# Kernel tuning notes

Hardware: AMD Instinct MI355X
Metric: run time of the kernel (lower is better)

Reference implementation:

```python
import jax, jax.numpy as jnp
import numpy as np

TEMPERATURE = 0.07
EPS = 1e-12


def setup_inputs() -> dict:
    key = jax.random.key(0)
    k1, k2 = jax.random.split(key)
    B, D = 16384, 256
    return {
        "query_embeds": jax.random.normal(k1, (B, D), dtype=jnp.float32),
        "database_embeds": jax.random.normal(k2, (B, D), dtype=jnp.float32),
    }


def _l2_normalize(x, axis=1):
    # torch F.normalize: x / max(||x||, eps)
    norm = jnp.sqrt(jnp.sum(x * x, axis=axis, keepdims=True))
    return x / jnp.maximum(norm, EPS)


def reference(query_embeds, database_embeds):
    q = _l2_normalize(query_embeds, axis=1)   # [B, D]
    d = _l2_normalize(database_embeds, axis=1)  # [B, D]
    sim = jnp.einsum("bd,cd->bc", q, d) / TEMPERATURE  # [B, B]
    B = sim.shape[0]
    diag = jnp.diagonal(sim)  # logits at the correct (matching) label
    # CE over rows (q->d): -log_softmax(sim, axis=1)[i, i]
    lse_rows = jax.nn.logsumexp(sim, axis=1)
    loss_q2d = jnp.mean(lse_rows - diag)
    # CE over rows of sim.T == columns of sim (d->q)
    lse_cols = jax.nn.logsumexp(sim, axis=0)
    loss_d2q = jnp.mean(lse_cols - diag)
    return (loss_q2d + loss_d2q) / 2
```

## Files before the change

### kernel.cpp

```cpp
#include <hip/hip_runtime.h>
#include <hip/hip_bf16.h>
#include <cstdint>
#include <cstddef>

#define B_ROWS 16384
#define D_DIM  256
#define TEMP_INV 14.285714285714286f

#define NITER 16

using frag_cd = __attribute__((ext_vector_type(4))) float;
using i32x4   = __attribute__((ext_vector_type(4))) int;
using i32x8   = __attribute__((ext_vector_type(8))) int;

__device__ __forceinline__ void gld_lds16(const void* g, void* l) {
    __builtin_amdgcn_global_load_lds(
        (const __attribute__((address_space(1))) void*)g,
        (__attribute__((address_space(3))) void*)l,
        16, 0, 0);
}


__global__ __launch_bounds__(256) void norm_diag_kernel(
    const float* __restrict__ q, const float* __restrict__ d,
    unsigned int* __restrict__ qn, unsigned int* __restrict__ dn,
    float* __restrict__ diag,
    float* __restrict__ row_sums, float* __restrict__ col_sums,
    float* __restrict__ out) {
    const int b = blockIdx.x;
    if (b < 64)            row_sums[b * 256 + threadIdx.x] = 0.0f;
    else if (b < 128)      col_sums[(b - 64) * 256 + threadIdx.x] = 0.0f;
    else if (b == 128 && threadIdx.x == 0) out[0] = 0.0f;

    const int t    = threadIdx.x;
    const int lane = t & 63;
    const int w    = t >> 6;
    const int l15  = lane & 15;
    const int rw   = lane >> 4;
    const int r    = w * 4 + rw;
    const int row  = b * 16 + r;

    const float4* qr = (const float4*)(q + (size_t)row * D_DIM);
    const float4* dr = (const float4*)(d + (size_t)row * D_DIM);
    float4 qv[4], dv[4];
    float qss = 0.f, dss = 0.f, qd = 0.f;
#pragma unroll
    for (int p = 0; p < 4; ++p) {
        qv[p] = qr[l15 + 16 * p];
        dv[p] = dr[l15 + 16 * p];
        qss += qv[p].x*qv[p].x + qv[p].y*qv[p].y + qv[p].z*qv[p].z + qv[p].w*qv[p].w;
        dss += dv[p].x*dv[p].x + dv[p].y*dv[p].y + dv[p].z*dv[p].z + dv[p].w*dv[p].w;
        qd  += qv[p].x*dv[p].x + qv[p].y*dv[p].y + qv[p].z*dv[p].z + qv[p].w*dv[p].w;
    }
#pragma unroll
    for (int off = 1; off < 16; off <<= 1) {
        qss += __shfl_xor(qss, off);
        dss += __shfl_xor(dss, off);
        qd  += __shfl_xor(qd,  off);
    }
    const float qinv = 1.0f / fmaxf(sqrtf(qss), 1e-12f);
    const float dinv = 1.0f / fmaxf(sqrtf(dss), 1e-12f);

    __shared__ unsigned int qbuf[1024], dbuf[1024];
#pragma unroll
    for (int p = 0; p < 4; ++p) {
        const int jw = l15 + 16 * p;
        int qp = 0, dp = 0;
        qp = __builtin_amdgcn_cvt_pk_fp8_f32(qv[p].x * qinv, qv[p].y * qinv, qp, false);
        qp = __builtin_amdgcn_cvt_pk_fp8_f32(qv[p].z * qinv, qv[p].w * qinv, qp, true);
        dp = __builtin_amdgcn_cvt_pk_fp8_f32(dv[p].x * dinv, dv[p].y * dinv, dp, false);
        dp = __builtin_amdgcn_cvt_pk_fp8_f32(dv[p].z * dinv, dv[p].w * dinv, dp, true);
        const int c    = (jw & 31) >> 2;
        const int widx = ((jw >> 5) << 9) | ((c >> 2) << 8) | ((c & 3) << 6)
                       | (r << 2) | (jw & 3);
        qbuf[widx] = (unsigned int)qp;
        dbuf[widx] = (unsigned int)dp;
    }
    if (l15 == 0) diag[row] = qd * qinv * dinv * TEMP_INV;
    __syncthreads();
    ((uint4*)qn)[(size_t)b * 256 + t] = ((const uint4*)qbuf)[t];
    ((uint4*)dn)[(size_t)b * 256 + t] = ((const uint4*)dbuf)[t];
}

__global__ __launch_bounds__(256, 2) void gemm_lse_kernel(
    const unsigned char* __restrict__ qn, const unsigned char* __restrict__ dn,
    float* __restrict__ row_sums, float* __restrict__ col_sums) {
    __shared__ unsigned char ldsB[3][16384];

    const int t    = threadIdx.x;
    const int lane = t & 63;
    const int w    = t >> 6;
    const int l15  = lane & 15;
    const int quad = lane >> 4;

    const int id   = blockIdx.x;
    const int xcd  = id & 7;
    const int i    = id >> 3;
    const int chunk   = (xcd << 1) | (i & 1);
    const int rowg    = i >> 1;
    const int rowBase = rowg * 256;
    const int colChunkBase = chunk * 1024;

    union OpU { i32x8 v; i32x4 h[2]; };

    const unsigned char* aB = qn + ((size_t)((rowBase >> 4) + w * 4) << 12) + lane * 16;
    OpU a8[4][2];
#pragma unroll
    for (int mi = 0; mi < 4; ++mi)
#pragma unroll
        for (int kt = 0; kt < 2; ++kt) {
            a8[mi][kt].h[0] = *(const i32x4*)(aB + mi * 4096 + kt * 2048);
            a8[mi][kt].h[1] = *(const i32x4*)(aB + mi * 4096 + kt * 2048 + 1024);
        }

    const unsigned char* bG = dn + ((size_t)(colChunkBase >> 4) << 12);

#define STAGE(bufidx, j)                                                      \
    {                                                                          \
        const unsigned char* gsrc = bG + (size_t)(j) * 16384;                  \
        unsigned char* ldst = &ldsB[bufidx][0];                                \
        _Pragma("unroll")                                                      \
        for (int ii = 0; ii < 4; ++ii)                                         \
            gld_lds16(gsrc + ii * 4096 + t * 16, ldst + ii * 4096 + t * 16);   \
    }

    STAGE(0, 0)
    STAGE(1, 1)

    union RV { frag_cd v[4]; float f[16]; } rvu;
#pragma unroll
    for (int k = 0; k < 4; ++k) rvu.v[k] = (frag_cd){0.f, 0.f, 0.f, 0.f};

    const float C2 = TEMP_INV * 1.44269504088896f;

    int cur = 0;
#pragma unroll 1
    for (int it = 0; it < NITER; ++it) {
        if (it == NITER - 1) asm volatile("s_waitcnt vmcnt(0)" ::: "memory");
        else                 asm volatile("s_waitcnt vmcnt(4)" ::: "memory");
        __builtin_amdgcn_s_barrier();
        asm volatile("" ::: "memory");

        const int nxt = (cur + 2 >= 3) ? cur - 1 : cur + 2;
        if (it + 2 < NITER) STAGE(nxt, it + 2)

        const unsigned char* bL = &ldsB[cur][0] + lane * 16;

        frag_cd acc[4][4];
#pragma unroll
        for (int mi = 0; mi < 4; ++mi)
#pragma unroll
            for (int ni = 0; ni < 4; ++ni)
                acc[mi][ni] = (frag_cd){0.f, 0.f, 0.f, 0.f};

        {
            OpU b8[4];
#pragma unroll
            for (int ni = 0; ni < 4; ++ni) {
                b8[ni].h[0] = *(const i32x4*)(bL + ni * 4096);
                b8[ni].h[1] = *(const i32x4*)(bL + ni * 4096 + 1024);
            }
            __builtin_amdgcn_s_setprio(1);
#pragma unroll
            for (int mi = 0; mi < 4; ++mi)
#pragma unroll
                for (int ni = 0; ni < 4; ++ni)
                    acc[mi][ni] = __builtin_amdgcn_mfma_scale_f32_16x16x128_f8f6f4(
                        a8[mi][0].v, b8[ni].v, acc[mi][ni],
                        0, 0, 0, 0x7F7F7F7F, 0, 0x7F7F7F7F);
            __builtin_amdgcn_s_setprio(0);
        }
        {
            OpU b8[4];
#pragma unroll
            for (int ni = 0; ni < 4; ++ni) {
                b8[ni].h[0] = *(const i32x4*)(bL + ni * 4096 + 2048);
                b8[ni].h[1] = *(const i32x4*)(bL + ni * 4096 + 2048 + 1024);
            }
            __builtin_amdgcn_s_setprio(1);
#pragma unroll
            for (int mi = 0; mi < 4; ++mi)
#pragma unroll
                for (int ni = 0; ni < 4; ++ni)
                    acc[mi][ni] = __builtin_amdgcn_mfma_scale_f32_16x16x128_f8f6f4(
                        a8[mi][1].v, b8[ni].v, acc[mi][ni],
                        0, 0, 0, 0x7F7F7F7F, 0, 0x7F7F7F7F);
            __builtin_amdgcn_s_setprio(0);
        }

        frag_cd cv4[4];
#pragma unroll
        for (int k = 0; k < 4; ++k) cv4[k] = (frag_cd){0.f, 0.f, 0.f, 0.f};
#pragma unroll
        for (int mi = 0; mi < 4; ++mi)
#pragma unroll
            for (int ni = 0; ni < 4; ++ni) {
                const frag_cd tt = acc[mi][ni] * C2 - C2;
                frag_cd e;
#pragma unroll
                for (int rr = 0; rr < 4; ++rr) e[rr] = __builtin_amdgcn_exp2f(tt[rr]);
                rvu.v[mi] += e;
                cv4[ni]   += e;
            }
        float cv[4];
#pragma unroll
        for (int ni = 0; ni < 4; ++ni)
            cv[ni] = (cv4[ni][0] + cv4[ni][1]) + (cv4[ni][2] + cv4[ni][3]);

#pragma unroll
        for (int s = 0; s < 2; ++s) {
            const bool bb = (quad >> s) & 1;
#pragma unroll
            for (int k = 0; k < (2 >> s); ++k) {
                const float a0 = cv[2 * k], a1 = cv[2 * k + 1];
                const float keep = bb ? a1 : a0;
                const float send = bb ? a0 : a1;
                cv[k] = keep + __shfl_xor(send, 16 << s);
            }
        }
        atomicAdd(&col_sums[colChunkBase + it * 64 + quad * 16 + l15], cv[0]);

        cur = (cur + 1 >= 3) ? 0 : cur + 1;
    }
#undef STAGE

#pragma unroll
    for (int s = 0; s < 4; ++s) {
        const bool bb = (l15 >> s) & 1;
#pragma unroll
        for (int k = 0; k < (8 >> s); ++k) {
            const float a0 = rvu.f[2 * k], a1 = rvu.f[2 * k + 1];
            const float keep = bb ? a1 : a0;
            const float send = bb ? a0 : a1;
            rvu.f[k] = keep + __shfl_xor(send, 1 << s);
        }
    }
    atomicAdd(&row_sums[rowBase + w * 64 + (l15 >> 2) * 16 + quad * 4 + (l15 & 3)],
              rvu.f[0]);
}

__global__ __launch_bounds__(256) void finalize_kernel(
    const float* __restrict__ rs, const float* __restrict__ cs,
    const float* __restrict__ dg, float* __restrict__ out) {
    const int i = blockIdx.x * 256 + threadIdx.x;
    float s = logf(rs[i]) + logf(cs[i]) - 2.0f * dg[i];
#pragma unroll
    for (int off = 32; off; off >>= 1) s += __shfl_down(s, off);
    __shared__ float buf[4];
    if ((threadIdx.x & 63) == 0) buf[threadIdx.x >> 6] = s;
    __syncthreads();
    if (threadIdx.x == 0) {
        float tot = (buf[0] + buf[1] + buf[2] + buf[3]) / (2.0f * B_ROWS);
        if (blockIdx.x == 0) tot += TEMP_INV;
        atomicAdd(out, tot);
    }
}

extern "C" void kernel_launch(void* const* d_in, const int* in_sizes, int n_in,
                              void* d_out, int out_size, void* d_ws, size_t ws_size,
                              hipStream_t stream) {
    const float* q = (const float*)d_in[0];
    const float* d = (const float*)d_in[1];
    float* out = (float*)d_out;

    char* ws = (char*)d_ws;
    unsigned char* qn = (unsigned char*)ws;
    unsigned char* dn = qn + (size_t)B_ROWS * D_DIM;
    float* row_sums = (float*)(ws + 2 * (size_t)B_ROWS * D_DIM);
    float* col_sums = row_sums + B_ROWS;
    float* diag     = col_sums + B_ROWS;

    norm_diag_kernel<<<B_ROWS / 16, 256, 0, stream>>>(
        q, d, (unsigned int*)qn, (unsigned int*)dn, diag, row_sums, col_sums, out);
    gemm_lse_kernel<<<(B_ROWS / 256) * (B_ROWS / 1024), 256, 0, stream>>>(
        qn, dn, row_sums, col_sums);
    finalize_kernel<<<B_ROWS / 256, 256, 0, stream>>>(row_sums, col_sums, diag, out);
}
```

Before: 149.8 us.

## Halve GEMM row tile, double-buffer LDS, and raise occupancy to four blocks

```diff
diff --git a/kernel.cpp b/kernel.cpp
--- a/kernel.cpp
+++ b/kernel.cpp
@@ -82,10 +82,10 @@
     ((uint4*)dn)[(size_t)b * 256 + t] = ((const uint4*)dbuf)[t];
 }
 
-__global__ __launch_bounds__(256, 2) void gemm_lse_kernel(
+__global__ __launch_bounds__(256, 4) void gemm_lse_kernel(
     const unsigned char* __restrict__ qn, const unsigned char* __restrict__ dn,
     float* __restrict__ row_sums, float* __restrict__ col_sums) {
-    __shared__ unsigned char ldsB[3][16384];
+    __shared__ unsigned char ldsB[2][16384];
 
     const int t    = threadIdx.x;
     const int lane = t & 63;
@@ -98,15 +98,15 @@
     const int i    = id >> 3;
     const int chunk   = (xcd << 1) | (i & 1);
     const int rowg    = i >> 1;
-    const int rowBase = rowg * 256;
+    const int rowBase = rowg * 128;
     const int colChunkBase = chunk * 1024;
 
     union OpU { i32x8 v; i32x4 h[2]; };
 
-    const unsigned char* aB = qn + ((size_t)((rowBase >> 4) + w * 4) << 12) + lane * 16;
-    OpU a8[4][2];
-#pragma unroll
-    for (int mi = 0; mi < 4; ++mi)
+    const unsigned char* aB = qn + ((size_t)((rowBase >> 4) + w * 2) << 12) + lane * 16;
+    OpU a8[2][2];
+#pragma unroll
+    for (int mi = 0; mi < 2; ++mi)
 #pragma unroll
         for (int kt = 0; kt < 2; ++kt) {
             a8[mi][kt].h[0] = *(const i32x4*)(aB + mi * 4096 + kt * 2048);
@@ -125,74 +125,60 @@
     }
 
     STAGE(0, 0)
-    STAGE(1, 1)
-
-    union RV { frag_cd v[4]; float f[16]; } rvu;
-#pragma unroll
-    for (int k = 0; k < 4; ++k) rvu.v[k] = (frag_cd){0.f, 0.f, 0.f, 0.f};
+
+    union RV { frag_cd v[2]; float f[8]; } rvu;
+#pragma unroll
+    for (int k = 0; k < 2; ++k) rvu.v[k] = (frag_cd){0.f, 0.f, 0.f, 0.f};
 
     const float C2 = TEMP_INV * 1.44269504088896f;
+    const frag_cd zf = (frag_cd){0.f, 0.f, 0.f, 0.f};
 
     int cur = 0;
 #pragma unroll 1
     for (int it = 0; it < NITER; ++it) {
-        if (it == NITER - 1) asm volatile("s_waitcnt vmcnt(0)" ::: "memory");
-        else                 asm volatile("s_waitcnt vmcnt(4)" ::: "memory");
+        asm volatile("s_waitcnt vmcnt(0)" ::: "memory");
         __builtin_amdgcn_s_barrier();
         asm volatile("" ::: "memory");
-
-        const int nxt = (cur + 2 >= 3) ? cur - 1 : cur + 2;
-        if (it + 2 < NITER) STAGE(nxt, it + 2)
+        if (it + 1 < NITER) STAGE(cur ^ 1, it + 1)
 
         const unsigned char* bL = &ldsB[cur][0] + lane * 16;
 
-        frag_cd acc[4][4];
-#pragma unroll
-        for (int mi = 0; mi < 4; ++mi)
+        frag_cd acc[2][4];
+        OpU b8[4];
+
+#pragma unroll
+        for (int ni = 0; ni < 4; ++ni) {
+            b8[ni].h[0] = *(const i32x4*)(bL + ni * 4096);
+            b8[ni].h[1] = *(const i32x4*)(bL + ni * 4096 + 1024);
+        }
+        __builtin_amdgcn_s_setprio(1);
+#pragma unroll
+        for (int mi = 0; mi < 2; ++mi)
 #pragma unroll
             for (int ni = 0; ni < 4; ++ni)
-                acc[mi][ni] = (frag_cd){0.f, 0.f, 0.f, 0.f};
-
-        {
-            OpU b8[4];
-#pragma unroll
-            for (int ni = 0; ni < 4; ++ni) {
-                b8[ni].h[0] = *(const i32x4*)(bL + ni * 4096);
-                b8[ni].h[1] = *(const i32x4*)(bL + ni * 4096 + 1024);
-            }
-            __builtin_amdgcn_s_setprio(1);
-#pragma unroll
-            for (int mi = 0; mi < 4; ++mi)
-#pragma unroll
-                for (int ni = 0; ni < 4; ++ni)
-                    acc[mi][ni] = __builtin_amdgcn_mfma_scale_f32_16x16x128_f8f6f4(
-                        a8[mi][0].v, b8[ni].v, acc[mi][ni],
-                        0, 0, 0, 0x7F7F7F7F, 0, 0x7F7F7F7F);
-            __builtin_amdgcn_s_setprio(0);
-        }
-        {
-            OpU b8[4];
-#pragma unroll
-            for (int ni = 0; ni < 4; ++ni) {
-                b8[ni].h[0] = *(const i32x4*)(bL + ni * 4096 + 2048);
-                b8[ni].h[1] = *(const i32x4*)(bL + ni * 4096 + 2048 + 1024);
-            }
-            __builtin_amdgcn_s_setprio(1);
-#pragma unroll
-            for (int mi = 0; mi < 4; ++mi)
-#pragma unroll
-                for (int ni = 0; ni < 4; ++ni)
-                    acc[mi][ni] = __builtin_amdgcn_mfma_scale_f32_16x16x128_f8f6f4(
-                        a8[mi][1].v, b8[ni].v, acc[mi][ni],
-                        0, 0, 0, 0x7F7F7F7F, 0, 0x7F7F7F7F);
-            __builtin_amdgcn_s_setprio(0);
-        }
-
-        frag_cd cv4[4];
-#pragma unroll
-        for (int k = 0; k < 4; ++k) cv4[k] = (frag_cd){0.f, 0.f, 0.f, 0.f};
-#pragma unroll
-        for (int mi = 0; mi < 4; ++mi)
+                acc[mi][ni] = __builtin_amdgcn_mfma_scale_f32_16x16x128_f8f6f4(
+                    a8[mi][0].v, b8[ni].v, zf,
+                    0, 0, 0, 0x7F7F7F7F, 0, 0x7F7F7F7F);
+        __builtin_amdgcn_s_setprio(0);
+
+#pragma unroll
+        for (int ni = 0; ni < 4; ++ni) {
+            b8[ni].h[0] = *(const i32x4*)(bL + ni * 4096 + 2048);
+            b8[ni].h[1] = *(const i32x4*)(bL + ni * 4096 + 2048 + 1024);
+        }
+        __builtin_amdgcn_s_setprio(1);
+#pragma unroll
+        for (int mi = 0; mi < 2; ++mi)
+#pragma unroll
+            for (int ni = 0; ni < 4; ++ni)
+                acc[mi][ni] = __builtin_amdgcn_mfma_scale_f32_16x16x128_f8f6f4(
+                    a8[mi][1].v, b8[ni].v, acc[mi][ni],
+                    0, 0, 0, 0x7F7F7F7F, 0, 0x7F7F7F7F);
+        __builtin_amdgcn_s_setprio(0);
+
+        float cv[4] = {0.f, 0.f, 0.f, 0.f};
+#pragma unroll
+        for (int mi = 0; mi < 2; ++mi)
 #pragma unroll
             for (int ni = 0; ni < 4; ++ni) {
                 const frag_cd tt = acc[mi][ni] * C2 - C2;
@@ -200,12 +186,8 @@
 #pragma unroll
                 for (int rr = 0; rr < 4; ++rr) e[rr] = __builtin_amdgcn_exp2f(tt[rr]);
                 rvu.v[mi] += e;
-                cv4[ni]   += e;
+                cv[ni] += (e[0] + e[1]) + (e[2] + e[3]);
             }
-        float cv[4];
-#pragma unroll
-        for (int ni = 0; ni < 4; ++ni)
-            cv[ni] = (cv4[ni][0] + cv4[ni][1]) + (cv4[ni][2] + cv4[ni][3]);
 
 #pragma unroll
         for (int s = 0; s < 2; ++s) {
@@ -220,23 +202,26 @@
         }
         atomicAdd(&col_sums[colChunkBase + it * 64 + quad * 16 + l15], cv[0]);
 
-        cur = (cur + 1 >= 3) ? 0 : cur + 1;
+        cur ^= 1;
     }
 #undef STAGE
 
 #pragma unroll
-    for (int s = 0; s < 4; ++s) {
+    for (int k = 0; k < 8; ++k) rvu.f[k] += __shfl_xor(rvu.f[k], 8);
+#pragma unroll
+    for (int s = 0; s < 3; ++s) {
         const bool bb = (l15 >> s) & 1;
 #pragma unroll
-        for (int k = 0; k < (8 >> s); ++k) {
+        for (int k = 0; k < (4 >> s); ++k) {
             const float a0 = rvu.f[2 * k], a1 = rvu.f[2 * k + 1];
             const float keep = bb ? a1 : a0;
             const float send = bb ? a0 : a1;
             rvu.f[k] = keep + __shfl_xor(send, 1 << s);
         }
     }
-    atomicAdd(&row_sums[rowBase + w * 64 + (l15 >> 2) * 16 + quad * 4 + (l15 & 3)],
-              rvu.f[0]);
+    if (l15 < 8)
+        atomicAdd(&row_sums[rowBase + w * 32 + ((l15 >> 2) & 1) * 16 + quad * 4
+                            + (l15 & 3)], rvu.f[0]);
 }
 
 __global__ __launch_bounds__(256) void finalize_kernel(
@@ -272,7 +257,7 @@
 
     norm_diag_kernel<<<B_ROWS / 16, 256, 0, stream>>>(
         q, d, (unsigned int*)qn, (unsigned int*)dn, diag, row_sums, col_sums, out);
-    gemm_lse_kernel<<<(B_ROWS / 256) * (B_ROWS / 1024), 256, 0, stream>>>(
+    gemm_lse_kernel<<<(B_ROWS / 128) * (B_ROWS / 1024), 256, 0, stream>>>(
         qn, dn, row_sums, col_sums);
     finalize_kernel<<<B_ROWS / 256, 256, 0, stream>>>(row_sums, col_sums, diag, out);
 }
```

New measurement: 160.5 us. +7.1%, slower.

## Switch B-tile staging to double buffering with staggered block start sleeps

Applied to the files above, without the earlier changes.

```diff
diff --git a/kernel.cpp b/kernel.cpp
--- a/kernel.cpp
+++ b/kernel.cpp
@@ -85,7 +85,7 @@
 __global__ __launch_bounds__(256, 2) void gemm_lse_kernel(
     const unsigned char* __restrict__ qn, const unsigned char* __restrict__ dn,
     float* __restrict__ row_sums, float* __restrict__ col_sums) {
-    __shared__ unsigned char ldsB[3][16384];
+    __shared__ unsigned char ldsB[2][16384];
 
     const int t    = threadIdx.x;
     const int lane = t & 63;
@@ -125,72 +125,63 @@
     }
 
     STAGE(0, 0)
-    STAGE(1, 1)
+    {
+        const int phase = (id >> 8) & 3;
+#pragma unroll 1
+        for (int p = 0; p < phase; ++p) __builtin_amdgcn_s_sleep(7);
+    }
 
     union RV { frag_cd v[4]; float f[16]; } rvu;
 #pragma unroll
     for (int k = 0; k < 4; ++k) rvu.v[k] = (frag_cd){0.f, 0.f, 0.f, 0.f};
 
     const float C2 = TEMP_INV * 1.44269504088896f;
+    const frag_cd zf = (frag_cd){0.f, 0.f, 0.f, 0.f};
 
     int cur = 0;
 #pragma unroll 1
     for (int it = 0; it < NITER; ++it) {
-        if (it == NITER - 1) asm volatile("s_waitcnt vmcnt(0)" ::: "memory");
-        else                 asm volatile("s_waitcnt vmcnt(4)" ::: "memory");
+        asm volatile("s_waitcnt vmcnt(0)" ::: "memory");
         __builtin_amdgcn_s_barrier();
         asm volatile("" ::: "memory");
-
-        const int nxt = (cur + 2 >= 3) ? cur - 1 : cur + 2;
-        if (it + 2 < NITER) STAGE(nxt, it + 2)
+        if (it + 1 < NITER) STAGE(cur ^ 1, it + 1)
 
         const unsigned char* bL = &ldsB[cur][0] + lane * 16;
 
         frag_cd acc[4][4];
+        OpU b8[4];
+
+#pragma unroll
+        for (int ni = 0; ni < 4; ++ni) {
+            b8[ni].h[0] = *(const i32x4*)(bL + ni * 4096);
+            b8[ni].h[1] = *(const i32x4*)(bL + ni * 4096 + 1024);
+        }
+        __builtin_amdgcn_s_setprio(1);
 #pragma unroll
         for (int mi = 0; mi < 4; ++mi)
 #pragma unroll
             for (int ni = 0; ni < 4; ++ni)
-                acc[mi][ni] = (frag_cd){0.f, 0.f, 0.f, 0.f};
-
-        {
-            OpU b8[4];
-#pragma unroll
-            for (int ni = 0; ni < 4; ++ni) {
-                b8[ni].h[0] = *(const i32x4*)(bL + ni * 4096);
-                b8[ni].h[1] = *(const i32x4*)(bL + ni * 4096 + 1024);
-            }
-            __builtin_amdgcn_s_setprio(1);
-#pragma unroll
-            for (int mi = 0; mi < 4; ++mi)
-#pragma unroll
-                for (int ni = 0; ni < 4; ++ni)
-                    acc[mi][ni] = __builtin_amdgcn_mfma_scale_f32_16x16x128_f8f6f4(
-                        a8[mi][0].v, b8[ni].v, acc[mi][ni],
-                        0, 0, 0, 0x7F7F7F7F, 0, 0x7F7F7F7F);
-            __builtin_amdgcn_s_setprio(0);
-        }
-        {
-            OpU b8[4];
-#pragma unroll
-            for (int ni = 0; ni < 4; ++ni) {
-                b8[ni].h[0] = *(const i32x4*)(bL + ni * 4096 + 2048);
-                b8[ni].h[1] = *(const i32x4*)(bL + ni * 4096 + 2048 + 1024);
-            }
-            __builtin_amdgcn_s_setprio(1);
-#pragma unroll
-            for (int mi = 0; mi < 4; ++mi)
-#pragma unroll
-                for (int ni = 0; ni < 4; ++ni)
-                    acc[mi][ni] = __builtin_amdgcn_mfma_scale_f32_16x16x128_f8f6f4(
-                        a8[mi][1].v, b8[ni].v, acc[mi][ni],
-                        0, 0, 0, 0x7F7F7F7F, 0, 0x7F7F7F7F);
-            __builtin_amdgcn_s_setprio(0);
-        }
-
-        frag_cd cv4[4];
-#pragma unroll
-        for (int k = 0; k < 4; ++k) cv4[k] = (frag_cd){0.f, 0.f, 0.f, 0.f};
+                acc[mi][ni] = __builtin_amdgcn_mfma_scale_f32_16x16x128_f8f6f4(
+                    a8[mi][0].v, b8[ni].v, zf,
+                    0, 0, 0, 0x7F7F7F7F, 0, 0x7F7F7F7F);
+        __builtin_amdgcn_s_setprio(0);
+
+#pragma unroll
+        for (int ni = 0; ni < 4; ++ni) {
+            b8[ni].h[0] = *(const i32x4*)(bL + ni * 4096 + 2048);
+            b8[ni].h[1] = *(const i32x4*)(bL + ni * 4096 + 2048 + 1024);
+        }
+        __builtin_amdgcn_s_setprio(1);
+#pragma unroll
+        for (int mi = 0; mi < 4; ++mi)
+#pragma unroll
+            for (int ni = 0; ni < 4; ++ni)
+                acc[mi][ni] = __builtin_amdgcn_mfma_scale_f32_16x16x128_f8f6f4(
+                    a8[mi][1].v, b8[ni].v, acc[mi][ni],
+                    0, 0, 0, 0x7F7F7F7F, 0, 0x7F7F7F7F);
+        __builtin_amdgcn_s_setprio(0);
+
+        float cv[4] = {0.f, 0.f, 0.f, 0.f};
 #pragma unroll
         for (int mi = 0; mi < 4; ++mi)
 #pragma unroll
@@ -200,12 +191,8 @@
 #pragma unroll
                 for (int rr = 0; rr < 4; ++rr) e[rr] = __builtin_amdgcn_exp2f(tt[rr]);
                 rvu.v[mi] += e;
-                cv4[ni]   += e;
+                cv[ni] += (e[0] + e[1]) + (e[2] + e[3]);
             }
-        float cv[4];
-#pragma unroll
-        for (int ni = 0; ni < 4; ++ni)
-            cv[ni] = (cv4[ni][0] + cv4[ni][1]) + (cv4[ni][2] + cv4[ni][3]);
 
 #pragma unroll
         for (int s = 0; s < 2; ++s) {
@@ -220,7 +207,7 @@
         }
         atomicAdd(&col_sums[colChunkBase + it * 64 + quad * 16 + l15], cv[0]);
 
-        cur = (cur + 1 >= 3) ? 0 : cur + 1;
+        cur ^= 1;
     }
 #undef STAGE
 
```

Result: slower. 157.6 us (+5.2%).
